# Performance work log

Measured on AMD Instinct MI355X. Metric: run time of the kernel, lower is better.

The kernel has to match this reference:

```python
import jax, jax.numpy as jnp
import numpy as np

# Fixed hyperparameters from init_kwargs
KH, KW = 3, 3
GRID_SIZE = 5
SPLINE_ORDER = 3
GRID_RANGE = (-1.0, 1.0)


def _make_grid():
    # grid buffer: arange(-k, grid_size + k + 1) * h + grid_range[0], shape (G + 2k + 1,) = (12,)
    h = (GRID_RANGE[1] - GRID_RANGE[0]) / GRID_SIZE
    return (jnp.arange(-SPLINE_ORDER, GRID_SIZE + SPLINE_ORDER + 1, dtype=jnp.float32) * h
            + GRID_RANGE[0])


def _unfold(x):
    # torch.nn.Unfold with kernel (3,3), stride 1, pad 0, dilation 1.
    # Returns (N, C*KH*KW) with channel-major ordering (c, i, j), matching torch.
    B, C, H, W = x.shape
    Ho, Wo = H - KH + 1, W - KW + 1
    cols = [x[:, :, i:i + Ho, j:j + Wo] for i in range(KH) for j in range(KW)]
    p = jnp.stack(cols, axis=2)                    # (B, C, KH*KW, Ho, Wo)
    p = p.reshape(B, C * KH * KW, Ho * Wo)         # (B, in_features, L)
    p = p.transpose(0, 2, 1).reshape(-1, C * KH * KW)  # (B*L, in_features)
    return p, Ho, Wo


def _b_splines(x, grid):
    # x: (N, in_features); grid: (G + 2k + 1,) uniform, shared across features.
    # Returns (N, in_features, G + k) B-spline basis via Cox-de Boor recursion.
    x = x[..., None]  # (N, in, 1)
    bases = ((x >= grid[:-1]) & (x < grid[1:])).astype(x.dtype)  # (N, in, G+2k)
    for k in range(1, SPLINE_ORDER + 1):
        left = (x - grid[: -(k + 1)]) / (grid[k:-1] - grid[: -(k + 1)])
        right = (grid[k + 1:] - x) / (grid[k + 1:] - grid[1:-k])
        bases = left * bases[..., :-1] + right * bases[..., 1:]
    return bases  # (N, in, G + k)


def setup_inputs() -> dict:
    key = jax.random.key(0)
    k1, k2, k3, k4 = jax.random.split(key, 4)
    in_features = 32 * KH * KW  # 288
    out_features = 64
    n_coef = GRID_SIZE + SPLINE_ORDER  # 8
    x = jax.random.normal(k1, (16, 32, 64, 64), dtype=jnp.float32)
    base_weight = jax.random.normal(k2, (out_features, in_features), dtype=jnp.float32) * (1.0 / np.sqrt(in_features))
    spline_weight = jax.random.normal(k3, (out_features, in_features, n_coef), dtype=jnp.float32) * 0.1
    spline_scaler = jax.random.normal(k4, (out_features, in_features), dtype=jnp.float32) * (1.0 / np.sqrt(in_features))
    return {"x": x, "base_weight": base_weight, "spline_weight": spline_weight,
            "spline_scaler": spline_scaler}


def reference(x, base_weight, spline_weight, spline_scaler):
    B = x.shape[0]
    out_features = base_weight.shape[0]
    grid = _make_grid()

    patches, Ho, Wo = _unfold(x)                              # (N, in_features)
    N, in_features = patches.shape

    # KANLinear forward
    base_out = jnp.matmul(jax.nn.relu(patches), base_weight.T)  # (N, out)
    bases = _b_splines(patches, grid)                           # (N, in, G+k)
    scaled_w = spline_weight * spline_scaler[..., None]         # (out, in, G+k)
    spline_out = jnp.matmul(bases.reshape(N, -1), scaled_w.reshape(out_features, -1).T)
    out = base_out + spline_out                                 # (N, out)

    out = out.reshape(B, Ho, Wo, out_features).transpose(0, 3, 1, 2)  # (B, C_out, Ho, Wo)
    return out
```

## Files before the change

kernel.cpp:

```cpp
#include <hip/hip_runtime.h>
#include <stdint.h>

typedef _Float16 half8  __attribute__((ext_vector_type(8)));
typedef float    f32x16 __attribute__((ext_vector_type(16)));
typedef uint32_t u32x4  __attribute__((ext_vector_type(4)));

#define NPIX 61504
#define LPB  3844
#define NOUT 64
#define NXPIX 2097152
#define BFRAG_BYTES 332800
#define PF 4


__device__ inline half8 bspline8(float xv) {
  float u = fmaf(xv, 2.5f, 5.5f);
  float fi = floorf(u);
  int i = (int)fi;
  float t = u - fi, s = 1.0f - t;
  float t2 = t * t, t3 = t2 * t;
  float s2 = s * s, s3 = s2 * s;
  float w3 = t3 * 0.16666667f;
  float w0 = s3 * 0.16666667f;
  float w1 = fmaf(0.5f, t3, -t2) + 0.66666667f;
  float w2 = fmaf(0.5f, s3, -s2) + 0.66666667f;
  uint32_t u01 = __builtin_bit_cast(uint32_t, __builtin_amdgcn_cvt_pkrtz(w0, w1));
  uint32_t u23 = __builtin_bit_cast(uint32_t, __builtin_amdgcn_cvt_pkrtz(w2, w3));
  uint64_t V = (uint64_t)u01 | ((uint64_t)u23 << 32);
  uint32_t vl = (uint32_t)(V << 16);
  u32x4 fr;
#pragma unroll
  for (int q = 0; q < 4; ++q) {
    int d = i - 2 * q;
    uint32_t rr = (uint32_t)(V >> ((48 - 16 * d) & 63));
    fr[q] = ((uint32_t)d <= 3u) ? rr : ((d == 4) ? vl : 0u);
  }
  return __builtin_bit_cast(half8, fr);
}

__global__ void prep_all(const float* __restrict__ x,
                         const float* __restrict__ bw,
                         const float* __restrict__ sw,
                         const float* __restrict__ sc,
                         half8* __restrict__ bsp,
                         half8* __restrict__ wt) {
  int bid = blockIdx.x;
  if (bid < 8192) {
    int i = bid * 256 + threadIdx.x;
    bsp[i] = bspline8(x[i]);
    return;
  }
  int t = (bid - 8192) * 256 + threadIdx.x;
  half8 v;
  int fi, h, o;
  if (t < 64 * 288) {
    o = t / 288;
    int f = t - o * 288;
    float scale = sc[t];
    const float* p = sw + t * 8;
#pragma unroll
    for (int j = 0; j < 8; ++j) v[j] = (_Float16)(p[j] * scale);
    int c  = (f * 57) >> 9;
    int r  = f - c * 9;
    int i2 = (r * 11) >> 5;
    int j2 = r - i2 * 3;
    int st = (i2 * 3 + j2) * 16 + (c >> 1);
    h  = c & 1;
    fi = st * 2 + (o >> 5);
  } else {
    int t2 = t - 64 * 288;
    o = t2 / 36;
    int g8 = t2 - o * 36;
    const float* p = bw + o * 288 + g8 * 8;
#pragma unroll
    for (int j = 0; j < 8; ++j) v[j] = (_Float16)p[j];
    int stb = g8 >> 1;
    h  = g8 & 1;
    fi = (144 + stb) * 2 + (o >> 5);
  }
  wt[fi * 64 + h * 32 + (o & 31)] = v;
}

__device__ inline void stage(const half8* __restrict__ s, half8* d,
                             int n128, int tid) {
  int wv = tid >> 6, lane = tid & 63;
  for (int it = 0; it < n128; ++it) {
    int off = it * 128 + wv * 64;
#if __has_builtin(__builtin_amdgcn_global_load_lds)
    __builtin_amdgcn_global_load_lds(
        (const __attribute__((address_space(1))) uint32_t*)(s + off + lane),
        (__attribute__((address_space(3))) uint32_t*)(d + off),
        16, 0, 0);
#else
    d[off + lane] = s[off + lane];
#endif
  }
}

__global__ __launch_bounds__(128, 2) void kan_main4(
    const float* __restrict__ x,
    const half8* __restrict__ bsp,
    const half8* __restrict__ wt,
    float* __restrict__ out) {
  __shared__ half8 smw[2][2304];

  const int tid  = threadIdx.x;
  const int lane = tid & 63;
  const int wv   = tid >> 6;
  const int l31  = lane & 31;
  const int h    = lane >> 5;

  int bid  = blockIdx.x;
  int tile = (bid < 480) ? ((bid & 7) * 60 + (bid >> 3)) : 480;
  const int pxw = tile * 128 + wv * 64;

  int xb[2];
#pragma unroll
  for (int np = 0; np < 2; ++np) {
    int p = pxw + np * 32 + l31;
    if (p > NPIX - 1) p = NPIX - 1;
    int b  = p / LPB;
    int l  = p - b * LPB;
    int ho = l / 62;
    int wo = l - ho * 62;
    xb[np] = b * 131072 + ho * 64 + wo;
  }

  f32x16 acc[2][2];
#pragma unroll
  for (int mo = 0; mo < 2; ++mo)
#pragma unroll
    for (int np = 0; np < 2; ++np)
#pragma unroll
      for (int i = 0; i < 16; ++i) acc[mo][np][i] = 0.f;

  stage(wt, &smw[0][0], 16, tid);

  const half8* pb0 = bsp + xb[0] + h * 4096;
  const half8* pb1 = bsp + xb[1] + h * 4096;
  half8 b0r[PF], b1r[PF];
#pragma unroll
  for (int p = 0; p < PF; ++p) {
    b0r[p] = pb0[p * 8192];
    b1r[p] = pb1[p * 8192];
  }

  int buf = 0;
  for (int ch = 0; ch < 9; ++ch) {
    __syncthreads();
    if (ch < 8) stage(wt + (ch + 1) * 2048, &smw[buf ^ 1][0], 16, tid);
    else        stage(wt + 18432,           &smw[buf ^ 1][0], 18, tid);

    int i2n = ((ch + 1) * 11) >> 5;
    int j2n = (ch + 1) - i2n * 3;
    const half8* nb0 = bsp + xb[0] + h * 4096 + i2n * 64 + j2n;
    const half8* nb1 = bsp + xb[1] + h * 4096 + i2n * 64 + j2n;
    const half8* wb = &smw[buf][0];

#pragma unroll
    for (int stl = 0; stl < 16; ++stl) {
      const int slot = stl & (PF - 1);
      half8 b0 = b0r[slot], b1 = b1r[slot];
      if (stl + PF < 16) {
        b0r[slot] = pb0[(stl + PF) * 8192];
        b1r[slot] = pb1[(stl + PF) * 8192];
      } else {
        b0r[slot] = nb0[(stl + PF - 16) * 8192];
        b1r[slot] = nb1[(stl + PF - 16) * 8192];
      }
      half8 a0 = wb[stl * 128 + lane];
      half8 a1 = wb[stl * 128 + 64 + lane];
      acc[0][0] = __builtin_amdgcn_mfma_f32_32x32x16_f16(a0, b0, acc[0][0], 0, 0, 0);
      acc[0][1] = __builtin_amdgcn_mfma_f32_32x32x16_f16(a0, b1, acc[0][1], 0, 0, 0);
      acc[1][0] = __builtin_amdgcn_mfma_f32_32x32x16_f16(a1, b0, acc[1][0], 0, 0, 0);
      acc[1][1] = __builtin_amdgcn_mfma_f32_32x32x16_f16(a1, b1, acc[1][1], 0, 0, 0);
    }
    pb0 = nb0;
    pb1 = nb1;
    buf ^= 1;
  }

  __syncthreads();
  {
    const half8* wb = &smw[buf][0];
#pragma unroll
    for (int stb = 0; stb < 18; ++stb) {
      int fb0 = stb * 16 + h * 8;
      half8 bb[2];
#pragma unroll
      for (int np = 0; np < 2; ++np) {
        u32x4 pk;
#pragma unroll
        for (int jj = 0; jj < 4; ++jj) {
          float v0, v1;
          {
            int f = fb0 + jj * 2;
            int c = (f * 57) >> 9; int r = f - c * 9;
            int a = (r * 11) >> 5; int b2 = r - a * 3;
            v0 = fmaxf(x[xb[np] + c * 4096 + a * 64 + b2], 0.f);
          }
          {
            int f = fb0 + jj * 2 + 1;
            int c = (f * 57) >> 9; int r = f - c * 9;
            int a = (r * 11) >> 5; int b2 = r - a * 3;
            v1 = fmaxf(x[xb[np] + c * 4096 + a * 64 + b2], 0.f);
          }
          pk[jj] = __builtin_bit_cast(uint32_t, __builtin_amdgcn_cvt_pkrtz(v0, v1));
        }
        bb[np] = __builtin_bit_cast(half8, pk);
      }
      half8 a0 = wb[stb * 128 + lane];
      half8 a1 = wb[stb * 128 + 64 + lane];
      acc[0][0] = __builtin_amdgcn_mfma_f32_32x32x16_f16(a0, bb[0], acc[0][0], 0, 0, 0);
      acc[0][1] = __builtin_amdgcn_mfma_f32_32x32x16_f16(a0, bb[1], acc[0][1], 0, 0, 0);
      acc[1][0] = __builtin_amdgcn_mfma_f32_32x32x16_f16(a1, bb[0], acc[1][0], 0, 0, 0);
      acc[1][1] = __builtin_amdgcn_mfma_f32_32x32x16_f16(a1, bb[1], acc[1][1], 0, 0, 0);
    }
  }

#pragma unroll
  for (int np = 0; np < 2; ++np) {
    int p = pxw + np * 32 + l31;
    bool ok = p < NPIX;
    int pc = ok ? p : NPIX - 1;
    int b = pc / LPB;
    int l = pc - b * LPB;
    float* ob = out + b * (NOUT * LPB) + l;
#pragma unroll
    for (int mo = 0; mo < 2; ++mo)
#pragma unroll
      for (int rg = 0; rg < 16; ++rg) {
        int o = mo * 32 + (rg & 3) + 8 * (rg >> 2) + 4 * h;
        if (ok) ob[o * LPB] = acc[mo][np][rg];
      }
  }
}

extern "C" void kernel_launch(void* const* d_in, const int* in_sizes, int n_in,
                              void* d_out, int out_size, void* d_ws, size_t ws_size,
                              hipStream_t stream) {
  const float* x  = (const float*)d_in[0];
  const float* bw = (const float*)d_in[1];
  const float* sw = (const float*)d_in[2];
  const float* sc = (const float*)d_in[3];
  float* out = (float*)d_out;
  half8* wt  = (half8*)d_ws;
  half8* bsp = (half8*)((char*)d_ws + BFRAG_BYTES);

  prep_all<<<8192 + 81, 256, 0, stream>>>(x, bw, sw, sc, bsp, wt);
  kan_main4<<<481, 128, 0, stream>>>(x, bsp, wt, out);
}
```

Measured before the change: 132.9 us.

## Shrink per-wave pixel tile and run four waves per block

The main kernel now uses 256-thread blocks of four waves, each wave covering 32 pixels instead of 64, which halves the accumulator state per wave. The weight staging chunks in LDS shrink to 1024/768 entries so 18 spline chunks plus 3 base chunks are double-buffered, and the rolling B-operand prefetch is replaced by loading 8 fragments per chunk. The aim is higher occupancy and more latency hiding. In exchange, each LDS weight read now feeds only two MFMAs instead of four, there are more barriers, and the explicit cross-chunk prefetch is lost.

```diff
diff --git a/kernel.cpp b/kernel.cpp
--- a/kernel.cpp
+++ b/kernel.cpp
@@ -10,7 +10,6 @@
 #define NOUT 64
 #define NXPIX 2097152
 #define BFRAG_BYTES 332800
-#define PF 4
 
 
 __device__ inline half8 bspline8(float xv) {
@@ -81,11 +80,11 @@
   wt[fi * 64 + h * 32 + (o & 31)] = v;
 }
 
-__device__ inline void stage(const half8* __restrict__ s, half8* d,
-                             int n128, int tid) {
+__device__ inline void stage256(const half8* __restrict__ s, half8* d,
+                                int n, int tid) {
   int wv = tid >> 6, lane = tid & 63;
-  for (int it = 0; it < n128; ++it) {
-    int off = it * 128 + wv * 64;
+  for (int it = 0; it < n; it += 256) {
+    int off = it + wv * 64;
 #if __has_builtin(__builtin_amdgcn_global_load_lds)
     __builtin_amdgcn_global_load_lds(
         (const __attribute__((address_space(1))) uint32_t*)(s + off + lane),
@@ -97,12 +96,12 @@
   }
 }
 
-__global__ __launch_bounds__(128, 2) void kan_main4(
+__global__ __launch_bounds__(256, 4) void kan_main5(
     const float* __restrict__ x,
     const half8* __restrict__ bsp,
     const half8* __restrict__ wt,
     float* __restrict__ out) {
-  __shared__ half8 smw[2][2304];
+  __shared__ half8 smw[2][1024];
 
   const int tid  = threadIdx.x;
   const int lane = tid & 63;
@@ -112,115 +111,90 @@
 
   int bid  = blockIdx.x;
   int tile = (bid < 480) ? ((bid & 7) * 60 + (bid >> 3)) : 480;
-  const int pxw = tile * 128 + wv * 64;
-
-  int xb[2];
-#pragma unroll
-  for (int np = 0; np < 2; ++np) {
-    int p = pxw + np * 32 + l31;
+  const int pxw = tile * 128 + wv * 32;
+
+  int xb;
+  {
+    int p = pxw + l31;
     if (p > NPIX - 1) p = NPIX - 1;
     int b  = p / LPB;
     int l  = p - b * LPB;
     int ho = l / 62;
     int wo = l - ho * 62;
-    xb[np] = b * 131072 + ho * 64 + wo;
-  }
-
-  f32x16 acc[2][2];
+    xb = b * 131072 + ho * 64 + wo;
+  }
+
+  f32x16 acc[2];
 #pragma unroll
   for (int mo = 0; mo < 2; ++mo)
 #pragma unroll
-    for (int np = 0; np < 2; ++np)
-#pragma unroll
-      for (int i = 0; i < 16; ++i) acc[mo][np][i] = 0.f;
-
-  stage(wt, &smw[0][0], 16, tid);
-
-  const half8* pb0 = bsp + xb[0] + h * 4096;
-  const half8* pb1 = bsp + xb[1] + h * 4096;
-  half8 b0r[PF], b1r[PF];
-#pragma unroll
-  for (int p = 0; p < PF; ++p) {
-    b0r[p] = pb0[p * 8192];
-    b1r[p] = pb1[p * 8192];
-  }
+    for (int i = 0; i < 16; ++i) acc[mo][i] = 0.f;
+
+  stage256(wt, &smw[0][0], 1024, tid);
 
   int buf = 0;
-  for (int ch = 0; ch < 9; ++ch) {
+  for (int ch = 0; ch < 18; ++ch) {
     __syncthreads();
-    if (ch < 8) stage(wt + (ch + 1) * 2048, &smw[buf ^ 1][0], 16, tid);
-    else        stage(wt + 18432,           &smw[buf ^ 1][0], 18, tid);
-
-    int i2n = ((ch + 1) * 11) >> 5;
-    int j2n = (ch + 1) - i2n * 3;
-    const half8* nb0 = bsp + xb[0] + h * 4096 + i2n * 64 + j2n;
-    const half8* nb1 = bsp + xb[1] + h * 4096 + i2n * 64 + j2n;
+    if (ch < 17) stage256(wt + (ch + 1) * 1024, &smw[buf ^ 1][0], 1024, tid);
+    else         stage256(wt + 18432,           &smw[buf ^ 1][0],  768, tid);
+
+    int sp = ch >> 1;
+    int i2 = (sp * 11) >> 5;
+    int j2 = sp - i2 * 3;
+    const half8* bp = bsp + xb + h * 4096 + i2 * 64 + j2 + (ch & 1) * (8 * 8192);
     const half8* wb = &smw[buf][0];
 
-#pragma unroll
-    for (int stl = 0; stl < 16; ++stl) {
-      const int slot = stl & (PF - 1);
-      half8 b0 = b0r[slot], b1 = b1r[slot];
-      if (stl + PF < 16) {
-        b0r[slot] = pb0[(stl + PF) * 8192];
-        b1r[slot] = pb1[(stl + PF) * 8192];
-      } else {
-        b0r[slot] = nb0[(stl + PF - 16) * 8192];
-        b1r[slot] = nb1[(stl + PF - 16) * 8192];
-      }
+    half8 bv[8];
+#pragma unroll
+    for (int stl = 0; stl < 8; ++stl) bv[stl] = bp[stl * 8192];
+
+#pragma unroll
+    for (int stl = 0; stl < 8; ++stl) {
       half8 a0 = wb[stl * 128 + lane];
       half8 a1 = wb[stl * 128 + 64 + lane];
-      acc[0][0] = __builtin_amdgcn_mfma_f32_32x32x16_f16(a0, b0, acc[0][0], 0, 0, 0);
-      acc[0][1] = __builtin_amdgcn_mfma_f32_32x32x16_f16(a0, b1, acc[0][1], 0, 0, 0);
-      acc[1][0] = __builtin_amdgcn_mfma_f32_32x32x16_f16(a1, b0, acc[1][0], 0, 0, 0);
-      acc[1][1] = __builtin_amdgcn_mfma_f32_32x32x16_f16(a1, b1, acc[1][1], 0, 0, 0);
+      acc[0] = __builtin_amdgcn_mfma_f32_32x32x16_f16(a0, bv[stl], acc[0], 0, 0, 0);
+      acc[1] = __builtin_amdgcn_mfma_f32_32x32x16_f16(a1, bv[stl], acc[1], 0, 0, 0);
     }
-    pb0 = nb0;
-    pb1 = nb1;
     buf ^= 1;
   }
 
-  __syncthreads();
+  for (int cb = 0; cb < 3; ++cb) {
+    __syncthreads();
+    if (cb < 2) stage256(wt + 18432 + (cb + 1) * 768, &smw[buf ^ 1][0], 768, tid);
+    const half8* wb = &smw[buf][0];
+#pragma unroll
+    for (int stl = 0; stl < 6; ++stl) {
+      int stb = cb * 6 + stl;
+      int fb0 = stb * 16 + h * 8;
+      u32x4 pk;
+#pragma unroll
+      for (int jj = 0; jj < 4; ++jj) {
+        float v0, v1;
+        {
+          int f = fb0 + jj * 2;
+          int c = (f * 57) >> 9; int r = f - c * 9;
+          int a = (r * 11) >> 5; int b2 = r - a * 3;
+          v0 = fmaxf(x[xb + c * 4096 + a * 64 + b2], 0.f);
+        }
+        {
+          int f = fb0 + jj * 2 + 1;
+          int c = (f * 57) >> 9; int r = f - c * 9;
+          int a = (r * 11) >> 5; int b2 = r - a * 3;
+          v1 = fmaxf(x[xb + c * 4096 + a * 64 + b2], 0.f);
+        }
+        pk[jj] = __builtin_bit_cast(uint32_t, __builtin_amdgcn_cvt_pkrtz(v0, v1));
+      }
+      half8 bb = __builtin_bit_cast(half8, pk);
+      half8 a0 = wb[stl * 128 + lane];
+      half8 a1 = wb[stl * 128 + 64 + lane];
+      acc[0] = __builtin_amdgcn_mfma_f32_32x32x16_f16(a0, bb, acc[0], 0, 0, 0);
+      acc[1] = __builtin_amdgcn_mfma_f32_32x32x16_f16(a1, bb, acc[1], 0, 0, 0);
+    }
+    buf ^= 1;
+  }
+
   {
-    const half8* wb = &smw[buf][0];
-#pragma unroll
-    for (int stb = 0; stb < 18; ++stb) {
-      int fb0 = stb * 16 + h * 8;
-      half8 bb[2];
-#pragma unroll
-      for (int np = 0; np < 2; ++np) {
-        u32x4 pk;
-#pragma unroll
-        for (int jj = 0; jj < 4; ++jj) {
-          float v0, v1;
-          {
-            int f = fb0 + jj * 2;
-            int c = (f * 57) >> 9; int r = f - c * 9;
-            int a = (r * 11) >> 5; int b2 = r - a * 3;
-            v0 = fmaxf(x[xb[np] + c * 4096 + a * 64 + b2], 0.f);
-          }
-          {
-            int f = fb0 + jj * 2 + 1;
-            int c = (f * 57) >> 9; int r = f - c * 9;
-            int a = (r * 11) >> 5; int b2 = r - a * 3;
-            v1 = fmaxf(x[xb[np] + c * 4096 + a * 64 + b2], 0.f);
-          }
-          pk[jj] = __builtin_bit_cast(uint32_t, __builtin_amdgcn_cvt_pkrtz(v0, v1));
-        }
-        bb[np] = __builtin_bit_cast(half8, pk);
-      }
-      half8 a0 = wb[stb * 128 + lane];
-      half8 a1 = wb[stb * 128 + 64 + lane];
-      acc[0][0] = __builtin_amdgcn_mfma_f32_32x32x16_f16(a0, bb[0], acc[0][0], 0, 0, 0);
-      acc[0][1] = __builtin_amdgcn_mfma_f32_32x32x16_f16(a0, bb[1], acc[0][1], 0, 0, 0);
-      acc[1][0] = __builtin_amdgcn_mfma_f32_32x32x16_f16(a1, bb[0], acc[1][0], 0, 0, 0);
-      acc[1][1] = __builtin_amdgcn_mfma_f32_32x32x16_f16(a1, bb[1], acc[1][1], 0, 0, 0);
-    }
-  }
-
-#pragma unroll
-  for (int np = 0; np < 2; ++np) {
-    int p = pxw + np * 32 + l31;
+    int p = pxw + l31;
     bool ok = p < NPIX;
     int pc = ok ? p : NPIX - 1;
     int b = pc / LPB;
@@ -231,7 +205,7 @@
 #pragma unroll
       for (int rg = 0; rg < 16; ++rg) {
         int o = mo * 32 + (rg & 3) + 8 * (rg >> 2) + 4 * h;
-        if (ok) ob[o * LPB] = acc[mo][np][rg];
+        if (ok) ob[o * LPB] = acc[mo][rg];
       }
   }
 }
@@ -248,5 +222,5 @@
   half8* bsp = (half8*)((char*)d_ws + BFRAG_BYTES);
 
   prep_all<<<8192 + 81, 256, 0, stream>>>(x, bw, sw, sc, bsp, wt);
-  kan_main4<<<481, 128, 0, stream>>>(x, bsp, wt, out);
-}
+  kan_main5<<<481, 256, 0, stream>>>(x, bsp, wt, out);
+}
```

New measurement: 131.7 us. About the same (-0.9%).
